# Optimization experiments

Hardware: AMD Instinct MI355X
Metric: run time of the kernel (lower is better)

The kernel has to match this reference:

```python
import jax, jax.numpy as jnp
import numpy as np

DIM = 128
H = 4            # num_heads
HD = DIM // H    # head_dim = 32
NH = H // 2      # half heads
MAXD = 128       # rpe max_dist
SPAN = 2 * MAXD + 1
TABLE = SPAN * SPAN
LAMBDA_INIT = 0.8


def setup_inputs() -> dict:
    key = jax.random.key(0)
    ks = jax.random.split(key, 18)
    B, Nq, Nkv = 2, 2048, 4096
    n = jax.random.normal
    inp = {
        "x_q": n(ks[0], (B, Nq, DIM), dtype=jnp.float32),
        "x_kv": n(ks[1], (B, Nkv, DIM), dtype=jnp.float32),
        "coords_q": jax.random.randint(ks[2], (B, Nq, 2), 0, 256, dtype=jnp.int32),
        "coords_k": jax.random.randint(ks[3], (B, Nkv, 2), 0, 256, dtype=jnp.int32),
        "alpha_map": jax.random.uniform(ks[4], (B, Nq, 1), dtype=jnp.float32),
        # projection weights stored input-major: y = x @ W + b
        "Wq": n(ks[5], (DIM, DIM), dtype=jnp.float32) * 0.02,
        "bq": jnp.zeros((DIM,), jnp.float32),
        "Wk": n(ks[6], (DIM, DIM), dtype=jnp.float32) * 0.02,
        "bk": jnp.zeros((DIM,), jnp.float32),
        "Wv": n(ks[7], (DIM, DIM), dtype=jnp.float32) * 0.02,
        "bv": jnp.zeros((DIM,), jnp.float32),
        "lq1": n(ks[8], (NH, HD), dtype=jnp.float32) * 0.1,
        "lk1": n(ks[9], (NH, HD), dtype=jnp.float32) * 0.1,
        "lq2": n(ks[10], (NH, HD), dtype=jnp.float32) * 0.1,
        "lk2": n(ks[11], (NH, HD), dtype=jnp.float32) * 0.1,
        "rpe_table": n(ks[12], (TABLE, H), dtype=jnp.float32) * 0.02,
        "Wp": n(ks[13], (DIM, DIM), dtype=jnp.float32) * 0.02,
        "bp": jnp.zeros((DIM,), jnp.float32),
    }
    return inp


def reference(x_q, x_kv, coords_q, coords_k, alpha_map,
              Wq, bq, Wk, bk, Wv, bv,
              lq1, lk1, lq2, lk2, rpe_table, Wp, bp):
    B, Nq, C = x_q.shape
    Nkv = x_kv.shape[1]
    scale = HD ** -0.5

    def to_heads(x, W, b, n):
        return (x @ W + b).reshape(B, n, H, HD).transpose(0, 2, 1, 3)  # [B,H,n,hd]

    q = to_heads(x_q, Wq, bq, Nq)
    k = to_heads(x_kv, Wk, bk, Nkv)
    v = to_heads(x_kv, Wv, bv, Nkv)

    # relative position bias gather: [B,Nq,Nkv] indices into [TABLE,H]
    rel = coords_q[:, :, None, :] - coords_k[:, None, :, :] + MAXD
    rel = jnp.clip(rel, 0, 2 * MAXD)
    idx = rel[..., 0] * SPAN + rel[..., 1]
    bias = jnp.transpose(rpe_table[idx], (0, 3, 1, 2))  # [B,H,Nq,Nkv]

    scores = jnp.einsum('bhqd,bhkd->bhqk', q, k) * scale + bias
    probs = jax.nn.softmax(scores, axis=-1)
    x_std = jnp.einsum('bhqk,bhkd->bhqd', probs, v)

    lam = (jnp.exp(jnp.sum(lq1 * lk1, axis=-1))
           - jnp.exp(jnp.sum(lq2 * lk2, axis=-1)) + LAMBDA_INIT)  # [NH]
    attn_diff = probs[:, :NH] - lam[None, :, None, None] * probs[:, NH:]
    x_diff = jnp.einsum('bhqk,bhkd->bhqd', attn_diff, v[:, :NH])

    x1 = x_std[:, :NH] + alpha_map[:, None, :, :] * x_diff  # alpha gating
    x = jnp.concatenate([x1, x_std[:, NH:]], axis=1)        # [B,H,Nq,hd]
    x = x.transpose(0, 2, 1, 3).reshape(B, Nq, C)
    return x @ Wp + bp
```

## Files before the change

### kernel.cpp

```cpp
#include <hip/hip_runtime.h>
#include <hip/hip_bf16.h>

#define B_ 2
#define H_ 4
#define HD_ 32
#define NQ_ 2048
#define NKV_ 4096
#define DIM_ 128
#define SPAN_ 257
#define TABLE_ 66049
#define SCALE_ 0.17677669529663687f
#define LAMBDA_INIT_ 0.8f
#define DTHR 4.0f
#define CAPR 36

typedef float f32x4 __attribute__((ext_vector_type(4)));
typedef short s16x4 __attribute__((ext_vector_type(4)));
typedef short s16x8 __attribute__((ext_vector_type(8)));
typedef int   i32x4 __attribute__((ext_vector_type(4)));
typedef float fl4   __attribute__((ext_vector_type(4)));

static __device__ __forceinline__ unsigned short f2bf(float f) {
  unsigned u = __float_as_uint(f);
  u += 0x7FFFu + ((u >> 16) & 1u);
  return (unsigned short)(u >> 16);
}
static __device__ __forceinline__ unsigned cvtpk(float lo, float hi) {
  unsigned r;
  asm("v_cvt_pk_bf16_f32 %0, %1, %2" : "=v"(r) : "v"(lo), "v"(hi));
  return r;
}

__global__ __launch_bounds__(256) void prep(
    const int* __restrict__ cq, const int* __restrict__ ck,
    const float* __restrict__ rpe,
    int* __restrict__ cqs, int* __restrict__ cks,
    int* __restrict__ qperm, int* __restrict__ kperm,
    int* __restrict__ qrank, int* __restrict__ krank,
    uint2* __restrict__ rpeb) {
  const int tid = threadIdx.x;
  const int blk = blockIdx.x;
  if (blk >= 4) {
    int ci = (blk - 4) * 256 + tid;
    if (ci < TABLE_) {
      fl4 v = *(const fl4*)(rpe + 4 * ci);
      uint2 o;
      o.x = cvtpk(v[0], v[1]);
      o.y = cvtpk(v[2], v[3]);
      rpeb[ci] = o;
    }
    return;
  }
  const int b = blk >> 1;
  const bool isq = (blk & 1) == 0;
  const int N = isq ? NQ_ : NKV_;
  const int S = N >> 8;
  const int* src = (isq ? cq : ck) + b * N * 2;
  int* sc   = (isq ? cqs : cks) + b * N * 2;
  int* perm = (isq ? qperm : kperm) + b * N;
  int* rank = (isq ? qrank : krank) + b * N;

  __shared__ int xv[NKV_];
  __shared__ int hist[16][256];
  __shared__ int wavehist[4][256];
  __shared__ int pref[256];

  for (int i = tid; i < N; i += 256) xv[i] = src[2 * i];
  for (int i = tid; i < S * 256; i += 256) ((int*)hist)[i] = 0;
  __syncthreads();
  for (int s = 0; s < S; ++s) atomicAdd(&hist[s][xv[s * 256 + tid]], 1);
  __syncthreads();
  int tot = 0;
  for (int s = 0; s < S; ++s) tot += hist[s][tid];
  pref[tid] = tot;
  __syncthreads();
  if (tid == 0) {
    int run = 0;
    for (int i = 0; i < 256; ++i) { int t = pref[i]; pref[i] = run; run += t; }
  }
  __syncthreads();
  {
    int run = pref[tid];
    for (int s = 0; s < S; ++s) { int h = hist[s][tid]; hist[s][tid] = run; run += h; }
  }
  const int lane = tid & 63, w = tid >> 6;
  __syncthreads();
  for (int s = 0; s < S; ++s) {
    wavehist[w][lane] = 0; wavehist[w][64 + lane] = 0;
    wavehist[w][128 + lane] = 0; wavehist[w][192 + lane] = 0;
    int e = s * 256 + tid;
    int x = xv[e];
    unsigned long long m = ~0ull;
#pragma unroll
    for (int bit = 0; bit < 8; ++bit) {
      unsigned long long bl = __ballot((x >> bit) & 1);
      m &= ((x >> bit) & 1) ? bl : ~bl;
    }
    unsigned long long lt = (1ull << lane) - 1ull;
    int lrank = __popcll(m & lt);
    if ((m & lt) == 0ull) wavehist[w][x] = __popcll(m);
    __syncthreads();
    int offs = 0;
#pragma unroll
    for (int w2 = 0; w2 < 4; ++w2) if (w2 < w) offs += wavehist[w2][x];
    int r = hist[s][x] + offs + lrank;
    perm[r] = e;
    rank[e] = r;
    sc[2 * r] = x;
    sc[2 * r + 1] = src[2 * e + 1];
    __syncthreads();
  }
}

__global__ __launch_bounds__(256) void qkv8p(
    const float* __restrict__ xq, const float* __restrict__ xkv,
    const float* __restrict__ Wq, const float* __restrict__ bq,
    const float* __restrict__ Wk, const float* __restrict__ bk,
    const float* __restrict__ Wv, const float* __restrict__ bv,
    const int* __restrict__ qrank, const int* __restrict__ krank,
    unsigned short* __restrict__ Qb, unsigned short* __restrict__ Kb,
    unsigned short* __restrict__ Vsw) {
  const int idx = blockIdx.x;
  const bool isq = idx < 512;
  const int b  = isq ? (idx >> 8) : ((idx - 512) >> 9);
  const int n0 = isq ? ((idx & 255) * 8) : (((idx - 512) & 511) * 8);
  const float* xsrc = isq ? xq : xkv;
  const int nlen = isq ? NQ_ : NKV_;

  __shared__ __align__(16) float xr[8][DIM_];
  const int tid = threadIdx.x;
  {
    const float* xbase = xsrc + ((size_t)b * nlen + n0) * DIM_;
    int rr = tid >> 5, c4 = tid & 31;
    *(fl4*)&xr[rr][c4 * 4] = *(const fl4*)(xbase + rr * DIM_ + c4 * 4);
  }
  __syncthreads();

  if (isq) {
    const int j = tid & 127, rh = tid >> 7;
    float acc[4];
    float bb = bq[j];
#pragma unroll
    for (int rr = 0; rr < 4; ++rr) acc[rr] = bb;
    for (int i4 = 0; i4 < 32; ++i4) {
      const float* wp = &Wq[(4 * i4) * DIM_ + j];
      float w0 = wp[0], w1 = wp[DIM_], w2 = wp[2 * DIM_], w3 = wp[3 * DIM_];
#pragma unroll
      for (int rr = 0; rr < 4; ++rr) {
        fl4 x4 = *(const fl4*)&xr[4 * rh + rr][4 * i4];
        acc[rr] = fmaf(x4[3], w3, fmaf(x4[2], w2, fmaf(x4[1], w1, fmaf(x4[0], w0, acc[rr]))));
      }
    }
    int h = j >> 5, d = j & 31;
#pragma unroll
    for (int rr = 0; rr < 4; ++rr) {
      int rq = qrank[b * NQ_ + n0 + 4 * rh + rr];
      Qb[(((size_t)b * H_ + h) * NQ_ + rq) * HD_ + d] = f2bf(acc[rr]);
    }
  } else {
    const int half = tid >> 7, j = tid & 127;
    const float* W = half ? Wv : Wk;
    float bb = half ? bv[j] : bk[j];
    float acc[8];
#pragma unroll
    for (int rr = 0; rr < 8; ++rr) acc[rr] = bb;
    for (int i4 = 0; i4 < 32; ++i4) {
      const float* wp = &W[(4 * i4) * DIM_ + j];
      float w0 = wp[0], w1 = wp[DIM_], w2 = wp[2 * DIM_], w3 = wp[3 * DIM_];
#pragma unroll
      for (int rr = 0; rr < 8; ++rr) {
        fl4 x4 = *(const fl4*)&xr[rr][4 * i4];
        acc[rr] = fmaf(x4[3], w3, fmaf(x4[2], w2, fmaf(x4[1], w1, fmaf(x4[0], w0, acc[rr]))));
      }
    }
    int h = j >> 5, d = j & 31;
    if (half == 0) {
#pragma unroll
      for (int rr = 0; rr < 8; ++rr) {
        int rk = krank[b * NKV_ + n0 + rr];
        Kb[(((size_t)b * H_ + h) * NKV_ + rk) * HD_ + d] = f2bf(acc[rr]);
      }
    } else {
#pragma unroll
      for (int rr = 0; rr < 8; ++rr) {
        int rk = krank[b * NKV_ + n0 + rr];
        int blk32 = rk & ~31, j32 = rk & 31;
        int posb = (j32 < 16) ? 8 * (j32 >> 2) + (j32 & 3)
                              : 8 * ((j32 - 16) >> 2) + 4 + (j32 & 3);
        Vsw[(((size_t)b * H_ + h) * HD_ + d) * NKV_ + blk32 + posb] = f2bf(acc[rr]);
      }
    }
  }
}

__global__ __launch_bounds__(512) void attn_win(
    const unsigned short* __restrict__ Qg, const unsigned short* __restrict__ Kg,
    const unsigned short* __restrict__ Vg, const int* __restrict__ cqs,
    const int* __restrict__ cks, const int* __restrict__ qperm,
    const float* __restrict__ alpha, const uint2* __restrict__ rpeb,
    const float* __restrict__ rpe,
    const float* __restrict__ lq1, const float* __restrict__ lk1,
    const float* __restrict__ lq2, const float* __restrict__ lk2,
    const float* __restrict__ Wp, const float* __restrict__ bp,
    float* __restrict__ out) {

  const int tid = threadIdx.x;
  const int lane = tid & 63;
  const int wv = tid >> 6;
  const int qcol = lane & 15;
  const int g = lane >> 4;
  const int qt = blockIdx.x & 127;
  const int b = blockIdx.x >> 7;
  const int qg0 = qt * 16;

  __shared__ struct {
    union {
      float acc[3][8][16][36];
      float xq[16][128];
      uint2 wnd[CAPR * 257];
    } u;
    float mW[8][17];
    float lW[4][8][17];
    float wgt[8][17];
    float lam[2];
  } S;

  if (tid < 2) {
    float s1 = 0.f, s2 = 0.f;
    for (int d = 0; d < HD_; ++d) {
      s1 += lq1[tid * HD_ + d] * lk1[tid * HD_ + d];
      s2 += lq2[tid * HD_ + d] * lk2[tid * HD_ + d];
    }
    S.lam[tid] = __expf(s1) - __expf(s2) + LAMBDA_INIT_;
  }

  s16x8 qf[4];
#pragma unroll
  for (int h = 0; h < 4; ++h)
    qf[h] = *(const s16x8*)(Qg + (((size_t)b * H_ + h) * NQ_ + qg0 + qcol) * HD_ + 8 * g);

  const int2* cq2 = (const int2*)cqs + (size_t)b * NQ_;
  const int2* ck2 = (const int2*)cks + (size_t)b * NKV_;
  const int2 cqv = cq2[qg0 + qcol];
  const int qx = cqv.x + 128, qy = cqv.y + 128;
  const int qxminp = cq2[qg0].x + 128;
  const int qxmaxp = cq2[qg0 + 15].x + 128;

  const unsigned short* kb[4];
  const unsigned short* vp[4][2];
#pragma unroll
  for (int h = 0; h < 4; ++h) {
    kb[h] = Kg + (((size_t)b * H_ + h) * NKV_ + wv * 32) * HD_;
#pragma unroll
    for (int dt = 0; dt < 2; ++dt)
      vp[h][dt] = Vg + (((size_t)b * H_ + h) * HD_ + dt * 16 + qcol) * NKV_ + wv * 32 + 8 * g;
  }
  int koff[2];
#pragma unroll
  for (int t = 0; t < 2; ++t) koff[t] = (16 * t + qcol) * HD_ + 8 * g;

  const i32x4* ck4 = (const i32x4*)cks + (((size_t)b * NKV_ + wv * 32) >> 1);
  const fl4* __restrict__ rpe4 = (const fl4*)rpe;

  float m_run = -INFINITY;
  float l_run[4] = {0.f, 0.f, 0.f, 0.f};
  f32x4 z4 = {0.f, 0.f, 0.f, 0.f};
  f32x4 aS[4][2], aC[2][2];
#pragma unroll
  for (int h = 0; h < 4; ++h) { aS[h][0] = z4; aS[h][1] = z4; }
#pragma unroll
  for (int p = 0; p < 2; ++p) { aC[p][0] = z4; aC[p][1] = z4; }

  s16x8 kf[4][2], vf[4][2];
  i32x4 ckt[4];
  fl4 gB[8];

#define CKLD(ST) {                                                         \
    const int s_ = (ST);                                                   \
    _Pragma("unroll") for (int t = 0; t < 2; ++t)                          \
    _Pragma("unroll") for (int hf = 0; hf < 2; ++hf)                       \
      ckt[2 * t + hf] = ck4[s_ * 128 + 8 * t + 2 * g + hf];                \
  }
#define KLD(ST) {                                                          \
    const int s_ = (ST);                                                   \
    _Pragma("unroll") for (int h = 0; h < 4; ++h)                          \
    _Pragma("unroll") for (int t = 0; t < 2; ++t)                          \
      kf[h][t] = *(const s16x8*)(kb[h] + s_ * 256 * HD_ + koff[t]);        \
  }
#define VLD(ST) {                                                          \
    const int s_ = (ST);                                                   \
    _Pragma("unroll") for (int h = 0; h < 4; ++h)                          \
    _Pragma("unroll") for (int dt = 0; dt < 2; ++dt)                       \
      vf[h][dt] = *(const s16x8*)(vp[h][dt] + s_ * 256);                   \
  }
#define LGATH(DXLO, RR) {                                                  \
    _Pragma("unroll") for (int t = 0; t < 2; ++t)                          \
    _Pragma("unroll") for (int hf = 0; hf < 2; ++hf) {                     \
      i32x4 cc = ckt[2 * t + hf];                                          \
      _Pragma("unroll") for (int e = 0; e < 2; ++e) {                      \
        int dx = qx - cc[2 * e];     dx = dx < 0 ? 0 : (dx > 256 ? 256 : dx); \
        int dy = qy - cc[2 * e + 1]; dy = dy < 0 ? 0 : (dy > 256 ? 256 : dy); \
        int wr = dx - (DXLO);                                              \
        fl4 gg;                                                            \
        if (wr >= 0 && wr < (RR)) {                                        \
          uint2 wd = S.u.wnd[wr * 257 + dy];                               \
          gg[0] = __uint_as_float(wd.x << 16);                             \
          gg[1] = __uint_as_float(wd.x & 0xffff0000u);                     \
          gg[2] = __uint_as_float(wd.y << 16);                             \
          gg[3] = __uint_as_float(wd.y & 0xffff0000u);                     \
        } else {                                                           \
          gg = rpe4[dx * SPAN_ + dy];                                      \
        }                                                                  \
        gB[4 * t + 2 * hf + e] = gg;                                       \
      }                                                                    \
    }                                                                      \
  }

  CKLD(0);
  KLD(0);

  for (int s = 0; s < 16; ++s) {
    int2 kmn = ck2[s * 256];
    int2 kmx = ck2[s * 256 + 255];
    int dxlo = qxminp - kmx.x; dxlo = dxlo < 0 ? 0 : (dxlo > 256 ? 256 : dxlo);
    int dxhi = qxmaxp - kmn.x; dxhi = dxhi < 0 ? 0 : (dxhi > 256 ? 256 : dxhi);
    int R = dxhi - dxlo + 1; if (R > CAPR) R = CAPR;
    __syncthreads();
    for (int i = tid; i < R * 257; i += 512) {
      int r = i / 257;
      S.u.wnd[i] = rpeb[(dxlo + r) * 257 + (i - r * 257)];
    }
    __syncthreads();

    f32x4 s0[4], s1[4];
#pragma unroll
    for (int h = 0; h < 4; ++h) {
      s0[h] = __builtin_amdgcn_mfma_f32_16x16x32_bf16(kf[h][0], qf[h], z4, 0, 0, 0);
      s1[h] = __builtin_amdgcn_mfma_f32_16x16x32_bf16(kf[h][1], qf[h], z4, 0, 0, 0);
    }
    VLD(s);
    KLD(s + 1 < 16 ? s + 1 : 15);
    LGATH(dxlo, R);

    float sv[4][8];
    float mx = -INFINITY;
#pragma unroll
    for (int h = 0; h < 4; ++h) {
#pragma unroll
      for (int r = 0; r < 4; ++r) {
        sv[h][r]     = fmaf(s0[h][r], SCALE_, gB[r][h]);
        sv[h][4 + r] = fmaf(s1[h][r], SCALE_, gB[4 + r][h]);
        mx = fmaxf(mx, fmaxf(sv[h][r], sv[h][4 + r]));
      }
    }
    mx = fmaxf(mx, __shfl_xor(mx, 16));
    mx = fmaxf(mx, __shfl_xor(mx, 32));
    if (__any(mx > m_run + DTHR)) {
      float mnew = fmaxf(m_run, mx);
      float fold = __expf(m_run - mnew);
      float fr[4];
#pragma unroll
      for (int r = 0; r < 4; ++r) fr[r] = __shfl(fold, 4 * g + r);
#pragma unroll
      for (int h = 0; h < 4; ++h) {
        l_run[h] *= fold;
#pragma unroll
        for (int dt = 0; dt < 2; ++dt)
#pragma unroll
          for (int r = 0; r < 4; ++r) aS[h][dt][r] *= fr[r];
      }
#pragma unroll
      for (int p = 0; p < 2; ++p)
#pragma unroll
        for (int dt = 0; dt < 2; ++dt)
#pragma unroll
          for (int r = 0; r < 4; ++r) aC[p][dt][r] *= fr[r];
      m_run = mnew;
    }
    s16x8 pa[4];
#pragma unroll
    for (int h = 0; h < 4; ++h) {
      float p[8], psum = 0.f;
#pragma unroll
      for (int ss = 0; ss < 8; ++ss) { p[ss] = __expf(sv[h][ss] - m_run); psum += p[ss]; }
      l_run[h] += psum;
      i32x4 pw;
#pragma unroll
      for (int c = 0; c < 4; ++c) pw[c] = (int)cvtpk(p[2 * c], p[2 * c + 1]);
      pa[h] = __builtin_bit_cast(s16x8, pw);
    }
    CKLD(s + 1 < 16 ? s + 1 : 15);

#pragma unroll
    for (int h = 0; h < 4; ++h)
#pragma unroll
      for (int dt = 0; dt < 2; ++dt)
        aS[h][dt] = __builtin_amdgcn_mfma_f32_16x16x32_bf16(pa[h], vf[h][dt], aS[h][dt], 0, 0, 0);
#pragma unroll
    for (int p = 0; p < 2; ++p)
#pragma unroll
      for (int dt = 0; dt < 2; ++dt)
        aC[p][dt] = __builtin_amdgcn_mfma_f32_16x16x32_bf16(pa[p + 2], vf[p][dt], aC[p][dt], 0, 0, 0);
  }

#pragma unroll
  for (int h = 0; h < 4; ++h) {
    l_run[h] += __shfl_xor(l_run[h], 16);
    l_run[h] += __shfl_xor(l_run[h], 32);
  }
  if (lane < 16) {
    S.mW[wv][lane] = m_run;
#pragma unroll
    for (int h = 0; h < 4; ++h) S.lW[h][wv][lane] = l_run[h];
  }
  __syncthreads();
  if (tid < 128) {
    int w = tid >> 4, q = tid & 15;
    float M = -INFINITY;
#pragma unroll
    for (int w2 = 0; w2 < 8; ++w2) M = fmaxf(M, S.mW[w2][q]);
    S.wgt[w][q] = __expf(S.mW[w][q] - M);
  }
  __syncthreads();

#pragma unroll
  for (int p = 0; p < 3; ++p)
#pragma unroll
    for (int dt = 0; dt < 2; ++dt)
#pragma unroll
      for (int r = 0; r < 4; ++r)
        S.u.acc[p][wv][4 * g + r][dt * 16 + qcol] = aS[p][dt][r];
  __syncthreads();
  const int q = tid >> 5, d = tid & 31;
  float wg[8];
#pragma unroll
  for (int w = 0; w < 8; ++w) wg[w] = S.wgt[w][q];
  float sumA[3] = {0.f, 0.f, 0.f};
#pragma unroll
  for (int p = 0; p < 3; ++p)
#pragma unroll
    for (int w = 0; w < 8; ++w) sumA[p] = fmaf(wg[w], S.u.acc[p][w][q][d], sumA[p]);
  __syncthreads();

#pragma unroll
  for (int dt = 0; dt < 2; ++dt)
#pragma unroll
    for (int r = 0; r < 4; ++r) {
      S.u.acc[0][wv][4 * g + r][dt * 16 + qcol] = aS[3][dt][r];
      S.u.acc[1][wv][4 * g + r][dt * 16 + qcol] = aC[0][dt][r];
      S.u.acc[2][wv][4 * g + r][dt * 16 + qcol] = aC[1][dt][r];
    }
  __syncthreads();
  float sumB[3] = {0.f, 0.f, 0.f};
#pragma unroll
  for (int p = 0; p < 3; ++p)
#pragma unroll
    for (int w = 0; w < 8; ++w) sumB[p] = fmaf(wg[w], S.u.acc[p][w][q][d], sumB[p]);

  float L[4];
#pragma unroll
  for (int h = 0; h < 4; ++h) {
    float ssum = 0.f;
#pragma unroll
    for (int w = 0; w < 8; ++w) ssum = fmaf(S.lW[h][w][q], S.wgt[w][q], ssum);
    L[h] = ssum;
  }
  int aorig = qperm[b * NQ_ + qg0 + q];
  float a = alpha[(size_t)b * NQ_ + aorig];
  float lam0 = S.lam[0], lam1 = S.lam[1];
  float xv0 = (1.f + a) * sumA[0] / L[0] - a * lam0 * sumB[1] / L[2];
  float xv1 = (1.f + a) * sumA[1] / L[1] - a * lam1 * sumB[2] / L[3];
  float xv2 = sumA[2] / L[2];
  float xv3 = sumB[0] / L[3];

  __syncthreads();
  S.u.xq[q][d]      = xv0;
  S.u.xq[q][32 + d] = xv1;
  S.u.xq[q][64 + d] = xv2;
  S.u.xq[q][96 + d] = xv3;
  __syncthreads();

  {
    const int j = tid & 127, rg = tid >> 7;
    float ob[4];
    float bpj = bp[j];
#pragma unroll
    for (int rr = 0; rr < 4; ++rr) ob[rr] = bpj;
#pragma unroll 4
    for (int i = 0; i < DIM_; ++i) {
      float w = Wp[i * DIM_ + j];
#pragma unroll
      for (int rr = 0; rr < 4; ++rr) ob[rr] = fmaf(S.u.xq[4 * rg + rr][i], w, ob[rr]);
    }
#pragma unroll
    for (int rr = 0; rr < 4; ++rr) {
      int orow = qperm[b * NQ_ + qg0 + 4 * rg + rr];
      out[((size_t)b * NQ_ + orow) * DIM_ + j] = ob[rr];
    }
  }
}

extern "C" void kernel_launch(void* const* d_in, const int* in_sizes, int n_in,
                              void* d_out, int out_size, void* d_ws, size_t ws_size,
                              hipStream_t stream) {
  const float* x_q   = (const float*)d_in[0];
  const float* x_kv  = (const float*)d_in[1];
  const int*   cq    = (const int*)d_in[2];
  const int*   ckc   = (const int*)d_in[3];
  const float* alpha = (const float*)d_in[4];
  const float* Wq    = (const float*)d_in[5];
  const float* bq    = (const float*)d_in[6];
  const float* Wk    = (const float*)d_in[7];
  const float* bk    = (const float*)d_in[8];
  const float* Wv    = (const float*)d_in[9];
  const float* bv    = (const float*)d_in[10];
  const float* lq1   = (const float*)d_in[11];
  const float* lk1   = (const float*)d_in[12];
  const float* lq2   = (const float*)d_in[13];
  const float* lk2   = (const float*)d_in[14];
  const float* rpe   = (const float*)d_in[15];
  const float* Wp    = (const float*)d_in[16];
  const float* bp    = (const float*)d_in[17];
  float* out = (float*)d_out;

  char* w = (char*)d_ws;
  unsigned short* Qb   = (unsigned short*)w;
  unsigned short* Kb   = (unsigned short*)(w + 1048576);
  unsigned short* Vsw  = (unsigned short*)(w + 3145728);
  uint2*          rpeb = (uint2*)(w + 5242880);
  int* cqs   = (int*)(w + 6291456);
  int* cks   = (int*)(w + 6356992);
  int* qperm = (int*)(w + 6422528);
  int* kperm = (int*)(w + 6488064);
  int* qrank = (int*)(w + 6553600);
  int* krank = (int*)(w + 6619136);

  prep<<<dim3(263), dim3(256), 0, stream>>>(
      cq, ckc, rpe, cqs, cks, qperm, kperm, qrank, krank, rpeb);

  qkv8p<<<dim3(1536), dim3(256), 0, stream>>>(
      x_q, x_kv, Wq, bq, Wk, bk, Wv, bv, qrank, krank, Qb, Kb, Vsw);

  attn_win<<<dim3(B_ * (NQ_ / 16)), dim3(512), 0, stream>>>(
      Qb, Kb, Vsw, cqs, cks, qperm, alpha, rpeb, rpe,
      lq1, lk1, lq2, lk2, Wp, bp, out);
}
```

Measured before the change: 127.8 us.

## Gather inputs by permutation in QKV projection and tighten rpe window bounds

New measurement: 131.9 us. 1.03x slower.

```diff
diff --git a/kernel.cpp b/kernel.cpp
--- a/kernel.cpp
+++ b/kernel.cpp
@@ -12,7 +12,7 @@
 #define SCALE_ 0.17677669529663687f
 #define LAMBDA_INIT_ 0.8f
 #define DTHR 4.0f
-#define CAPR 36
+#define CAPR 28
 
 typedef float f32x4 __attribute__((ext_vector_type(4)));
 typedef short s16x4 __attribute__((ext_vector_type(4)));
@@ -112,12 +112,12 @@
   }
 }
 
-__global__ __launch_bounds__(256) void qkv8p(
+__global__ __launch_bounds__(256) void qkv8g(
     const float* __restrict__ xq, const float* __restrict__ xkv,
     const float* __restrict__ Wq, const float* __restrict__ bq,
     const float* __restrict__ Wk, const float* __restrict__ bk,
     const float* __restrict__ Wv, const float* __restrict__ bv,
-    const int* __restrict__ qrank, const int* __restrict__ krank,
+    const int* __restrict__ qperm, const int* __restrict__ kperm,
     unsigned short* __restrict__ Qb, unsigned short* __restrict__ Kb,
     unsigned short* __restrict__ Vsw) {
   const int idx = blockIdx.x;
@@ -125,14 +125,16 @@
   const int b  = isq ? (idx >> 8) : ((idx - 512) >> 9);
   const int n0 = isq ? ((idx & 255) * 8) : (((idx - 512) & 511) * 8);
   const float* xsrc = isq ? xq : xkv;
+  const int* perm = (isq ? qperm + b * NQ_ : kperm + b * NKV_);
   const int nlen = isq ? NQ_ : NKV_;
 
   __shared__ __align__(16) float xr[8][DIM_];
   const int tid = threadIdx.x;
   {
-    const float* xbase = xsrc + ((size_t)b * nlen + n0) * DIM_;
     int rr = tid >> 5, c4 = tid & 31;
-    *(fl4*)&xr[rr][c4 * 4] = *(const fl4*)(xbase + rr * DIM_ + c4 * 4);
+    int orig = perm[n0 + rr];
+    *(fl4*)&xr[rr][c4 * 4] =
+        *(const fl4*)(xsrc + ((size_t)b * nlen + orig) * DIM_ + c4 * 4);
   }
   __syncthreads();
 
@@ -152,11 +154,9 @@
       }
     }
     int h = j >> 5, d = j & 31;
-#pragma unroll
-    for (int rr = 0; rr < 4; ++rr) {
-      int rq = qrank[b * NQ_ + n0 + 4 * rh + rr];
-      Qb[(((size_t)b * H_ + h) * NQ_ + rq) * HD_ + d] = f2bf(acc[rr]);
-    }
+    unsigned short* qb = Qb + (((size_t)b * H_ + h) * NQ_ + n0 + 4 * rh) * HD_ + d;
+#pragma unroll
+    for (int rr = 0; rr < 4; ++rr) qb[rr * HD_] = f2bf(acc[rr]);
   } else {
     const int half = tid >> 7, j = tid & 127;
     const float* W = half ? Wv : Wk;
@@ -175,19 +175,20 @@
     }
     int h = j >> 5, d = j & 31;
     if (half == 0) {
-#pragma unroll
-      for (int rr = 0; rr < 8; ++rr) {
-        int rk = krank[b * NKV_ + n0 + rr];
-        Kb[(((size_t)b * H_ + h) * NKV_ + rk) * HD_ + d] = f2bf(acc[rr]);
-      }
+      unsigned short* kb2 = Kb + (((size_t)b * H_ + h) * NKV_ + n0) * HD_ + d;
+#pragma unroll
+      for (int rr = 0; rr < 8; ++rr) kb2[rr * HD_] = f2bf(acc[rr]);
     } else {
-#pragma unroll
-      for (int rr = 0; rr < 8; ++rr) {
-        int rk = krank[b * NKV_ + n0 + rr];
-        int blk32 = rk & ~31, j32 = rk & 31;
-        int posb = (j32 < 16) ? 8 * (j32 >> 2) + (j32 & 3)
-                              : 8 * ((j32 - 16) >> 2) + 4 + (j32 & 3);
-        Vsw[(((size_t)b * H_ + h) * HD_ + d) * NKV_ + blk32 + posb] = f2bf(acc[rr]);
+      unsigned short* vb = Vsw + (((size_t)b * H_ + h) * HD_ + d) * NKV_ + (n0 & ~31);
+      const int base = n0 & 31;
+#pragma unroll
+      for (int c = 0; c < 2; ++c) {
+        int k0r = base + 4 * c;
+        int posb = (k0r < 16) ? 8 * (k0r >> 2) : 8 * ((k0r - 16) >> 2) + 4;
+        s16x4 t4;
+#pragma unroll
+        for (int e = 0; e < 4; ++e) t4[e] = (short)f2bf(acc[4 * c + e]);
+        *(s16x4*)(vb + posb) = t4;
       }
     }
   }
@@ -223,6 +224,7 @@
     float lW[4][8][17];
     float wgt[8][17];
     float lam[2];
+    int kbmin[8], kbmax[8];
   } S;
 
   if (tid < 2) {
@@ -243,8 +245,14 @@
   const int2* ck2 = (const int2*)cks + (size_t)b * NKV_;
   const int2 cqv = cq2[qg0 + qcol];
   const int qx = cqv.x + 128, qy = cqv.y + 128;
-  const int qxminp = cq2[qg0].x + 128;
-  const int qxmaxp = cq2[qg0 + 15].x + 128;
+
+  int qminx = 1 << 30, qmaxx = -(1 << 30);
+#pragma unroll
+  for (int i = 0; i < 16; ++i) {
+    int xq_ = cq2[qg0 + i].x;
+    qminx = min(qminx, xq_);
+    qmaxx = max(qmaxx, xq_);
+  }
 
   const unsigned short* kb[4];
   const unsigned short* vp[4][2];
@@ -320,12 +328,23 @@
   KLD(0);
 
   for (int s = 0; s < 16; ++s) {
-    int2 kmn = ck2[s * 256];
-    int2 kmx = ck2[s * 256 + 255];
-    int dxlo = qxminp - kmx.x; dxlo = dxlo < 0 ? 0 : (dxlo > 256 ? 256 : dxlo);
-    int dxhi = qxmaxp - kmn.x; dxhi = dxhi < 0 ? 0 : (dxhi > 256 ? 256 : dxhi);
+    __syncthreads();
+    {
+      int mn = 1 << 30, mx = -(1 << 30);
+      if (tid < 256) { int xk = ck2[s * 256 + tid].x; mn = xk; mx = xk; }
+#pragma unroll
+      for (int o = 32; o; o >>= 1) {
+        mn = min(mn, __shfl_xor(mn, o));
+        mx = max(mx, __shfl_xor(mx, o));
+      }
+      if (lane == 0) { S.kbmin[wv] = mn; S.kbmax[wv] = mx; }
+    }
+    __syncthreads();
+    int kminx = min(min(S.kbmin[0], S.kbmin[1]), min(S.kbmin[2], S.kbmin[3]));
+    int kmaxx = max(max(S.kbmax[0], S.kbmax[1]), max(S.kbmax[2], S.kbmax[3]));
+    int dxlo = qminx + 128 - kmaxx; dxlo = dxlo < 0 ? 0 : (dxlo > 256 ? 256 : dxlo);
+    int dxhi = qmaxx + 128 - kminx; dxhi = dxhi < 0 ? 0 : (dxhi > 256 ? 256 : dxhi);
     int R = dxhi - dxlo + 1; if (R > CAPR) R = CAPR;
-    __syncthreads();
     for (int i = tid; i < R * 257; i += 512) {
       int r = i / 257;
       S.u.wnd[i] = rpeb[(dxlo + r) * 257 + (i - r * 257)];
@@ -343,20 +362,20 @@
     LGATH(dxlo, R);
 
     float sv[4][8];
-    float mx = -INFINITY;
+    float mx2 = -INFINITY;
 #pragma unroll
     for (int h = 0; h < 4; ++h) {
 #pragma unroll
       for (int r = 0; r < 4; ++r) {
         sv[h][r]     = fmaf(s0[h][r], SCALE_, gB[r][h]);
         sv[h][4 + r] = fmaf(s1[h][r], SCALE_, gB[4 + r][h]);
-        mx = fmaxf(mx, fmaxf(sv[h][r], sv[h][4 + r]));
+        mx2 = fmaxf(mx2, fmaxf(sv[h][r], sv[h][4 + r]));
       }
     }
-    mx = fmaxf(mx, __shfl_xor(mx, 16));
-    mx = fmaxf(mx, __shfl_xor(mx, 32));
-    if (__any(mx > m_run + DTHR)) {
-      float mnew = fmaxf(m_run, mx);
+    mx2 = fmaxf(mx2, __shfl_xor(mx2, 16));
+    mx2 = fmaxf(mx2, __shfl_xor(mx2, 32));
+    if (__any(mx2 > m_run + DTHR)) {
+      float mnew = fmaxf(m_run, mx2);
       float fold = __expf(m_run - mnew);
       float fr[4];
 #pragma unroll
@@ -538,8 +557,8 @@
   prep<<<dim3(263), dim3(256), 0, stream>>>(
       cq, ckc, rpe, cqs, cks, qperm, kperm, qrank, krank, rpeb);
 
-  qkv8p<<<dim3(1536), dim3(256), 0, stream>>>(
-      x_q, x_kv, Wq, bq, Wk, bk, Wv, bv, qrank, krank, Qb, Kb, Vsw);
+  qkv8g<<<dim3(1536), dim3(256), 0, stream>>>(
+      x_q, x_kv, Wq, bq, Wk, bk, Wv, bv, qperm, kperm, Qb, Kb, Vsw);
 
   attn_win<<<dim3(B_ * (NQ_ / 16)), dim3(512), 0, stream>>>(
       Qb, Kb, Vsw, cqs, cks, qperm, alpha, rpeb, rpe,
```
